# Performance work log

Hardware: AMD Instinct MI355X
Metric: run time of the kernel (lower is better)

## Reference

```python
import jax, jax.numpy as jnp
import numpy as np

DELTA = 0.1
NEG_INF = -1e30


def setup_inputs() -> dict:
    key = jax.random.key(0)
    k1, k2, k3, k4 = jax.random.split(key, 4)
    Bs, Bt, D, C = 8192, 8192, 64, 10
    return {
        "src_feas": jax.random.normal(k1, (Bs, D), dtype=jnp.float32),
        "src_labels": jax.random.randint(k2, (Bs,), 0, C, dtype=jnp.int32),
        "tgt_feas": jax.random.normal(k3, (Bt, D), dtype=jnp.float32),
        "tgt_logits": jax.random.normal(k4, (Bt, C), dtype=jnp.float32),
    }


def reference(src_feas, src_labels, tgt_feas, tgt_logits):
    # The original builds the explicit list of positive pairs (i_tgt, j_src)
    # where tgt sample i is 'confident' (top1-top2 logit gap >= delta) and
    # src_labels[j] == argmax(tgt_logits[i]).  The [P, P] score matrix it
    # forms is s[k, l] = src_feas[j_k] . tgt_feas[i_l], which only depends on
    # (j_k, i_l), so sum(diag(log_softmax(s))) collapses to a weighted
    # logsumexp over the [Bs, Bt] cross-domain score matrix. Same math,
    # fully vectorized, order-invariant.
    Bs = src_feas.shape[0]
    C = tgt_logits.shape[1]

    top2 = jax.lax.top_k(tgt_logits, 2)[0]                  # [Bt, 2]
    conf = (top2[:, 0] - top2[:, 1]) >= DELTA               # [Bt]
    cls = jnp.argmax(tgt_logits, axis=1)                    # [Bt]

    # per-class count of source samples
    counts = jnp.zeros((C,), jnp.float32).at[src_labels].add(1.0)  # [C]
    # w[i] = multiplicity of tgt sample i in the pair list
    w = jnp.where(conf, counts[cls], 0.0)                   # [Bt]

    M = src_feas @ tgt_feas.T                               # [Bs, Bt]
    logw = jnp.where(w > 0, jnp.log(jnp.maximum(w, 1.0)), NEG_INF)
    # L[j] = log sum over all pairs l of exp(M[j, i_l])
    L = jax.scipy.special.logsumexp(M + logw[None, :], axis=1)  # [Bs]

    pair_mask = conf[None, :] & (src_labels[:, None] == cls[None, :])  # [Bs, Bt]
    nce_sum = jnp.sum(jnp.where(pair_mask, M - L[:, None], 0.0))
    P = jnp.sum(w)                                          # total pair count
    nce = nce_sum / (-1.0 * Bs * P)
    return nce
```

## Files before the change

kernel.cpp:

```cpp
#include <hip/hip_runtime.h>
#include <hip/hip_bf16.h>

#define BSZ 8192
#define BTZ 8192
#define DD 64
#define NC 10
#define SHIFT2 20.0f
#define LN2 0.69314718055994531f
#define LOG2E 1.44269504088896341f

typedef __attribute__((ext_vector_type(8))) short bf16x8;
typedef __attribute__((ext_vector_type(4))) float f32x4;

#if defined(__has_builtin)
#if __has_builtin(__builtin_amdgcn_exp2f)
#define EXP2(x) __builtin_amdgcn_exp2f(x)
#else
#define EXP2(x) exp2f(x)
#endif
#else
#define EXP2(x) exp2f(x)
#endif

__device__ __forceinline__ unsigned short f2bf_rne(float f) {
    unsigned int u = __float_as_uint(f);
    u += 0x7FFFu + ((u >> 16) & 1u);
    return (unsigned short)(u >> 16);
}

__global__ __launch_bounds__(256) void kAB(
    const float4* __restrict__ src4, const float4* __restrict__ tgt4,
    const int* __restrict__ labels, const float* __restrict__ logits,
    ushort4* __restrict__ srcb, ushort4* __restrict__ tgtb,
    float* __restrict__ S, float* __restrict__ counts,
    float* __restrict__ cc_part, unsigned char* __restrict__ cls8,
    float* __restrict__ cbias_c, int* __restrict__ cidx,
    int* __restrict__ gcursor)
{
    int t = threadIdx.x;
    if (blockIdx.x < 512) {
        int tid = blockIdx.x * 256 + t;
        float4 s = src4[tid];
        ushort4 os;
        os.x = f2bf_rne(s.x * LOG2E); os.y = f2bf_rne(s.y * LOG2E);
        os.z = f2bf_rne(s.z * LOG2E); os.w = f2bf_rne(s.w * LOG2E);
        srcb[tid] = os;
        float4 v = tgt4[tid];
        ushort4 ot; ot.x = f2bf_rne(v.x); ot.y = f2bf_rne(v.y);
        ot.z = f2bf_rne(v.z); ot.w = f2bf_rne(v.w);
        tgtb[tid] = ot;
        return;
    }
    __shared__ float lcnt[NC];
    __shared__ float hist[NC];
    __shared__ float hred[4][NC];
    __shared__ int lpos;
    __shared__ int lbase;
    int b = blockIdx.x - 512;
    int i = b * 256 + t;
    int w = t >> 6, lane = t & 63;

    float c10[NC];
    #pragma unroll
    for (int c = 0; c < NC; ++c) c10[c] = 0.0f;
    for (int k = 0; k < 32; ++k) {
        int lab = labels[t + 256 * k];
        #pragma unroll
        for (int c = 0; c < NC; ++c) c10[c] += (lab == c) ? 1.0f : 0.0f;
    }
    #pragma unroll
    for (int c = 0; c < NC; ++c) {
        float v = c10[c];
        #pragma unroll
        for (int m = 1; m < 64; m <<= 1) v += __shfl_xor(v, m);
        if (lane == 0) hred[w][c] = v;
    }
    if (t == 0) lpos = 0;
    if (t < NC) hist[t] = 0.0f;
    __syncthreads();
    if (t < NC) lcnt[t] = hred[0][t] + hred[1][t] + hred[2][t] + hred[3][t];
    __syncthreads();
    if (b == 0 && t < NC) counts[t] = lcnt[t];

    float m1 = -3.0e38f, m2 = -3.0e38f; int cls = 0;
    #pragma unroll
    for (int c = 0; c < NC; ++c) {
        float v = logits[i * NC + c];
        if (v > m1) { m2 = m1; m1 = v; cls = c; }
        else if (v > m2) { m2 = v; }
    }
    bool conf = (m1 - m2) >= 0.1f;
    float cnt = lcnt[cls];
    bool live = conf && (cnt > 0.0f);
    cls8[i] = live ? (unsigned char)cls : (unsigned char)255;
    S[i] = 0.0f;
    if (conf) atomicAdd(&hist[cls], 1.0f);
    int myp = 0;
    if (live) myp = atomicAdd(&lpos, 1);
    __syncthreads();
    if (t < NC) cc_part[b * NC + t] = hist[t];
    if (t == 0) lbase = atomicAdd(gcursor, lpos);
    __syncthreads();
    if (live) {
        cidx[lbase + myp] = i;
        cbias_c[lbase + myp] = log2f(cnt) - SHIFT2;
    }
}

__global__ __launch_bounds__(256) void kC(
    const unsigned short* __restrict__ srcb, const unsigned short* __restrict__ tgtb,
    const float* __restrict__ cbias_c, const int* __restrict__ cidx,
    const int* __restrict__ gcursor, float* __restrict__ S,
    const float* __restrict__ srcf, const float* __restrict__ tgtf,
    const int* __restrict__ labels, const unsigned char* __restrict__ cls8,
    float* __restrict__ SC, float* __restrict__ T)
{
    int t = threadIdx.x;
    if (blockIdx.x >= 2048) {
        int bb = blockIdx.x - 2048;
        bool isT = bb >= 32;
        int rb = (bb & 31) * 256;
        const float* F = isT ? tgtf : srcf;
        int w = t >> 6, lane = t & 63;
        float acc[NC];
        #pragma unroll
        for (int c = 0; c < NC; ++c) acc[c] = 0.0f;
        int row0 = rb + w * 64;
        for (int r = 0; r < 64; ++r) {
            int row = row0 + r;
            int lab = isT ? (int)cls8[row] : labels[row];
            float f = F[row * DD + lane];
            #pragma unroll
            for (int c = 0; c < NC; ++c) acc[c] += (lab == c) ? f : 0.0f;
        }
        float* OUT = isT ? T : SC;
        #pragma unroll
        for (int c = 0; c < NC; ++c) atomicAdd(&OUT[c * DD + lane], acc[c]);
        return;
    }

    __shared__ float lds[4][64];
    int w = t >> 6;
    int lane = t & 63;
    int l15 = lane & 15;
    int quad = lane >> 4;
    int colchunk = blockIdx.x & 15;
    int rowg = blockIdx.x >> 4;
    int row_base = rowg * 64;
    int Pn = *gcursor;
    if (colchunk * 512 >= Pn) return;

    bf16x8 a[4][2];
    #pragma unroll
    for (int mb = 0; mb < 4; ++mb) {
        const bf16x8* p = (const bf16x8*)(srcb + (size_t)(row_base + mb * 16 + l15) * DD + quad * 8);
        a[mb][0] = p[0];
        a[mb][1] = p[4];
    }

    float rs[4][4];
    #pragma unroll
    for (int mb = 0; mb < 4; ++mb)
        #pragma unroll
        for (int r = 0; r < 4; ++r) rs[mb][r] = 0.0f;

    int col0 = colchunk * 512 + w * 128;
    #pragma unroll 2
    for (int ct = 0; ct < 8; ++ct) {
        int cb = col0 + ct * 16;
        int cc = cb + l15;
        bool ok = cc < Pn;
        int col = ok ? cidx[cc] : 0;
        float cb2 = ok ? cbias_c[cc] : -1.0e30f;
        const bf16x8* q = (const bf16x8*)(tgtb + (size_t)col * DD + quad * 8);
        bf16x8 b0 = q[0];
        bf16x8 b1 = q[4];
        #pragma unroll
        for (int mb = 0; mb < 4; ++mb) {
            f32x4 acc = {cb2, cb2, cb2, cb2};
            acc = __builtin_amdgcn_mfma_f32_16x16x32_bf16(a[mb][0], b0, acc, 0, 0, 0);
            acc = __builtin_amdgcn_mfma_f32_16x16x32_bf16(a[mb][1], b1, acc, 0, 0, 0);
            #pragma unroll
            for (int r = 0; r < 4; ++r)
                rs[mb][r] += EXP2(acc[r]);
        }
    }

    #pragma unroll
    for (int mb = 0; mb < 4; ++mb) {
        #pragma unroll
        for (int r = 0; r < 4; ++r) {
            float v = rs[mb][r];
            v += __shfl_xor(v, 1);
            v += __shfl_xor(v, 2);
            v += __shfl_xor(v, 4);
            v += __shfl_xor(v, 8);
            if (l15 == 0) lds[w][mb * 16 + quad * 4 + r] = v;
        }
    }
    __syncthreads();
    if (t < 64)
        atomicAdd(&S[row_base + t], lds[0][t] + lds[1][t] + lds[2][t] + lds[3][t]);
}

__global__ __launch_bounds__(256) void kD(
    const float* __restrict__ S, const int* __restrict__ labels,
    const float* __restrict__ counts, const float* __restrict__ cc_part,
    const float* __restrict__ SC, const float* __restrict__ T,
    float* __restrict__ gACC, int* __restrict__ gcnt,
    float* __restrict__ out)
{
    __shared__ float cc[NC];
    __shared__ float redL[4], red1[4], redP[4];
    __shared__ int isLast;
    int t = threadIdx.x;
    int w = t >> 6, lane = t & 63;
    if (t < NC) {
        float s = 0.0f;
        #pragma unroll
        for (int k = 0; k < 32; ++k) s += cc_part[k * NC + t];
        cc[t] = s;
    }
    __syncthreads();
    int j = blockIdx.x * 256 + t;
    float L = (log2f(S[j]) + SHIFT2) * LN2;
    float tl = cc[labels[j]] * L;
    #pragma unroll
    for (int m = 1; m < 64; m <<= 1) tl += __shfl_xor(tl, m);
    if (lane == 0) redL[w] = tl;
    __syncthreads();
    if (t == 0) {
        float v = redL[0] + redL[1] + redL[2] + redL[3];
        atomicAdd(&gACC[0], v);
        __threadfence();
        int old = atomicAdd(gcnt, 1);
        isLast = (old == 31) ? 1 : 0;
    }
    __syncthreads();
    if (!isLast) return;

    float t1 = 0.0f;
    for (int o = t; o < NC * DD; o += 256) t1 += SC[o] * T[o];
    float Pp = (t < NC) ? counts[t] * cc[t] : 0.0f;
    #pragma unroll
    for (int m = 1; m < 64; m <<= 1) {
        t1 += __shfl_xor(t1, m);
        Pp += __shfl_xor(Pp, m);
    }
    if (lane == 0) { red1[w] = t1; redP[w] = Pp; }
    __syncthreads();
    if (t == 0) {
        float term1 = red1[0] + red1[1] + red1[2] + red1[3];
        float P = redP[0] + redP[1] + redP[2] + redP[3];
        float termL = atomicAdd(&gACC[0], 0.0f);
        out[0] = (term1 - termL) / (-(float)BSZ * P);
    }
}

extern "C" void kernel_launch(void* const* d_in, const int* in_sizes, int n_in,
                              void* d_out, int out_size, void* d_ws, size_t ws_size,
                              hipStream_t stream) {
    const float* src    = (const float*)d_in[0];
    const int*   labels = (const int*)d_in[1];
    const float* tgt    = (const float*)d_in[2];
    const float* logits = (const float*)d_in[3];

    char* ws = (char*)d_ws;
    float* S        = (float*)(ws + 0);
    int*   gcursor  = (int*)(ws + 32768);
    int*   gcnt     = (int*)(ws + 32772);
    float* gACC     = (float*)(ws + 32776);
    float* counts   = (float*)(ws + 32784);
    float* cc_part  = (float*)(ws + 32832);
    float* SC       = (float*)(ws + 34112);
    float* T        = (float*)(ws + 36672);
    float* cbias_c  = (float*)(ws + 40960);
    int*   cidx     = (int*)(ws + 73728);
    unsigned char* cls8 = (unsigned char*)(ws + 106496);
    unsigned short* srcb = (unsigned short*)(ws + 114688);
    unsigned short* tgtb = (unsigned short*)(ws + 114688 + 1048576);

    hipMemsetAsync(ws + 32768, 0, 8192, stream);
    kAB<<<544, 256, 0, stream>>>((const float4*)src, (const float4*)tgt, labels,
                                 logits, (ushort4*)srcb, (ushort4*)tgtb,
                                 S, counts, cc_part, cls8, cbias_c, cidx, gcursor);
    kC<<<2112, 256, 0, stream>>>(srcb, tgtb, cbias_c, cidx, gcursor, S,
                                 src, tgt, labels, cls8, SC, T);
    kD<<<32, 256, 0, stream>>>(S, labels, counts, cc_part, SC, T,
                               gACC, gcnt, (float*)d_out);
}
```

Before: 122.1 us.

## Replace compacted column list with dense per-column bias masking in score kernel

Drops the atomic compaction of confident target indices and instead writes a per-column log2 bias for every target, using -1e30 for dead columns. The score kernel then walks all 8192 columns contiguously with no index gather, preloads its B fragments and biases up front, and halves the per-block column chunk, which doubles the grid. Launch bounds now request 4 blocks per CU. This removes the gather indirection, the global cursor read and the serial atomic cursor, but it evaluates exp2 on non-confident columns that were skipped before.

```diff
diff --git a/kernel.cpp b/kernel.cpp
--- a/kernel.cpp
+++ b/kernel.cpp
@@ -34,8 +34,7 @@
     ushort4* __restrict__ srcb, ushort4* __restrict__ tgtb,
     float* __restrict__ S, float* __restrict__ counts,
     float* __restrict__ cc_part, unsigned char* __restrict__ cls8,
-    float* __restrict__ cbias_c, int* __restrict__ cidx,
-    int* __restrict__ gcursor)
+    float* __restrict__ colbias)
 {
     int t = threadIdx.x;
     if (blockIdx.x < 512) {
@@ -54,8 +53,6 @@
     __shared__ float lcnt[NC];
     __shared__ float hist[NC];
     __shared__ float hred[4][NC];
-    __shared__ int lpos;
-    __shared__ int lbase;
     int b = blockIdx.x - 512;
     int i = b * 256 + t;
     int w = t >> 6, lane = t & 63;
@@ -75,7 +72,6 @@
         for (int m = 1; m < 64; m <<= 1) v += __shfl_xor(v, m);
         if (lane == 0) hred[w][c] = v;
     }
-    if (t == 0) lpos = 0;
     if (t < NC) hist[t] = 0.0f;
     __syncthreads();
     if (t < NC) lcnt[t] = hred[0][t] + hred[1][t] + hred[2][t] + hred[3][t];
@@ -92,32 +88,24 @@
     bool conf = (m1 - m2) >= 0.1f;
     float cnt = lcnt[cls];
     bool live = conf && (cnt > 0.0f);
+    colbias[i] = live ? (log2f(cnt) - SHIFT2) : -1.0e30f;
     cls8[i] = live ? (unsigned char)cls : (unsigned char)255;
     S[i] = 0.0f;
     if (conf) atomicAdd(&hist[cls], 1.0f);
-    int myp = 0;
-    if (live) myp = atomicAdd(&lpos, 1);
     __syncthreads();
     if (t < NC) cc_part[b * NC + t] = hist[t];
-    if (t == 0) lbase = atomicAdd(gcursor, lpos);
-    __syncthreads();
-    if (live) {
-        cidx[lbase + myp] = i;
-        cbias_c[lbase + myp] = log2f(cnt) - SHIFT2;
-    }
-}
-
-__global__ __launch_bounds__(256) void kC(
+}
+
+__global__ __launch_bounds__(256, 4) void kC(
     const unsigned short* __restrict__ srcb, const unsigned short* __restrict__ tgtb,
-    const float* __restrict__ cbias_c, const int* __restrict__ cidx,
-    const int* __restrict__ gcursor, float* __restrict__ S,
+    const float* __restrict__ colbias, float* __restrict__ S,
     const float* __restrict__ srcf, const float* __restrict__ tgtf,
     const int* __restrict__ labels, const unsigned char* __restrict__ cls8,
     float* __restrict__ SC, float* __restrict__ T)
 {
     int t = threadIdx.x;
-    if (blockIdx.x >= 2048) {
-        int bb = blockIdx.x - 2048;
+    if (blockIdx.x >= 4096) {
+        int bb = blockIdx.x - 4096;
         bool isT = bb >= 32;
         int rb = (bb & 31) * 256;
         const float* F = isT ? tgtf : srcf;
@@ -144,11 +132,9 @@
     int lane = t & 63;
     int l15 = lane & 15;
     int quad = lane >> 4;
-    int colchunk = blockIdx.x & 15;
-    int rowg = blockIdx.x >> 4;
+    int colchunk = blockIdx.x & 31;
+    int rowg = blockIdx.x >> 5;
     int row_base = rowg * 64;
-    int Pn = *gcursor;
-    if (colchunk * 512 >= Pn) return;
 
     bf16x8 a[4][2];
     #pragma unroll
@@ -157,6 +143,17 @@
         a[mb][0] = p[0];
         a[mb][1] = p[4];
     }
+    int col0 = colchunk * 256 + w * 64;
+    bf16x8 b[4][2];
+    float cb2[4];
+    #pragma unroll
+    for (int ct = 0; ct < 4; ++ct) {
+        int cc = col0 + ct * 16 + l15;
+        const bf16x8* q = (const bf16x8*)(tgtb + (size_t)cc * DD + quad * 8);
+        b[ct][0] = q[0];
+        b[ct][1] = q[4];
+        cb2[ct] = colbias[cc];
+    }
 
     float rs[4][4];
     #pragma unroll
@@ -164,22 +161,13 @@
         #pragma unroll
         for (int r = 0; r < 4; ++r) rs[mb][r] = 0.0f;
 
-    int col0 = colchunk * 512 + w * 128;
-    #pragma unroll 2
-    for (int ct = 0; ct < 8; ++ct) {
-        int cb = col0 + ct * 16;
-        int cc = cb + l15;
-        bool ok = cc < Pn;
-        int col = ok ? cidx[cc] : 0;
-        float cb2 = ok ? cbias_c[cc] : -1.0e30f;
-        const bf16x8* q = (const bf16x8*)(tgtb + (size_t)col * DD + quad * 8);
-        bf16x8 b0 = q[0];
-        bf16x8 b1 = q[4];
+    #pragma unroll
+    for (int ct = 0; ct < 4; ++ct) {
         #pragma unroll
         for (int mb = 0; mb < 4; ++mb) {
-            f32x4 acc = {cb2, cb2, cb2, cb2};
-            acc = __builtin_amdgcn_mfma_f32_16x16x32_bf16(a[mb][0], b0, acc, 0, 0, 0);
-            acc = __builtin_amdgcn_mfma_f32_16x16x32_bf16(a[mb][1], b1, acc, 0, 0, 0);
+            f32x4 acc = {cb2[ct], cb2[ct], cb2[ct], cb2[ct]};
+            acc = __builtin_amdgcn_mfma_f32_16x16x32_bf16(a[mb][0], b[ct][0], acc, 0, 0, 0);
+            acc = __builtin_amdgcn_mfma_f32_16x16x32_bf16(a[mb][1], b[ct][1], acc, 0, 0, 0);
             #pragma unroll
             for (int r = 0; r < 4; ++r)
                 rs[mb][r] += EXP2(acc[r]);
@@ -267,24 +255,22 @@
 
     char* ws = (char*)d_ws;
     float* S        = (float*)(ws + 0);
-    int*   gcursor  = (int*)(ws + 32768);
-    int*   gcnt     = (int*)(ws + 32772);
+    int*   gcnt     = (int*)(ws + 32768);
     float* gACC     = (float*)(ws + 32776);
     float* counts   = (float*)(ws + 32784);
     float* cc_part  = (float*)(ws + 32832);
     float* SC       = (float*)(ws + 34112);
     float* T        = (float*)(ws + 36672);
-    float* cbias_c  = (float*)(ws + 40960);
-    int*   cidx     = (int*)(ws + 73728);
-    unsigned char* cls8 = (unsigned char*)(ws + 106496);
-    unsigned short* srcb = (unsigned short*)(ws + 114688);
-    unsigned short* tgtb = (unsigned short*)(ws + 114688 + 1048576);
+    float* colbias  = (float*)(ws + 40960);
+    unsigned char* cls8 = (unsigned char*)(ws + 73728);
+    unsigned short* srcb = (unsigned short*)(ws + 81920);
+    unsigned short* tgtb = (unsigned short*)(ws + 81920 + 1048576);
 
     hipMemsetAsync(ws + 32768, 0, 8192, stream);
     kAB<<<544, 256, 0, stream>>>((const float4*)src, (const float4*)tgt, labels,
                                  logits, (ushort4*)srcb, (ushort4*)tgtb,
-                                 S, counts, cc_part, cls8, cbias_c, cidx, gcursor);
-    kC<<<2112, 256, 0, stream>>>(srcb, tgtb, cbias_c, cidx, gcursor, S,
+                                 S, counts, cc_part, cls8, colbias);
+    kC<<<4160, 256, 0, stream>>>(srcb, tgtb, colbias, S,
                                  src, tgt, labels, cls8, SC, T);
     kD<<<32, 256, 0, stream>>>(S, labels, counts, cc_part, SC, T,
                                gACC, gcnt, (float*)d_out);
```

New measurement: 123.9 us. About the same (+1.4%).

## Fuse finalization into GEMM kernel and compute positive-pair term from MFMA scores

Applied to the files above, without the earlier changes.

Removes the compacted confident-column list and instead runs the bf16 MFMA logsumexp over all 8192 target columns, masking dead columns with a large negative bias stored alongside the class in a packed per-column metadata array. The positive-pair sum is accumulated inside the MFMA loop by comparing row labels to column classes, which replaces the separate class-sum feature reduction blocks. The final reduction now runs in the last-finishing block of the GEMM kernel, which drops the third launch and the memset. In exchange every column is always computed, so the early-exit skip for chunks beyond the live count is gone, the inner loop gains a compare and add per element, and the positive term now uses bf16 scores with a bias correction instead of fp32 feature sums.

```diff
diff --git a/kernel.cpp b/kernel.cpp
--- a/kernel.cpp
+++ b/kernel.cpp
@@ -33,9 +33,8 @@
     const int* __restrict__ labels, const float* __restrict__ logits,
     ushort4* __restrict__ srcb, ushort4* __restrict__ tgtb,
     float* __restrict__ S, float* __restrict__ counts,
-    float* __restrict__ cc_part, unsigned char* __restrict__ cls8,
-    float* __restrict__ cbias_c, int* __restrict__ cidx,
-    int* __restrict__ gcursor)
+    float* __restrict__ cc_part, int2* __restrict__ colmeta,
+    int* __restrict__ gcnt, float* __restrict__ gACC)
 {
     int t = threadIdx.x;
     if (blockIdx.x < 512) {
@@ -54,8 +53,6 @@
     __shared__ float lcnt[NC];
     __shared__ float hist[NC];
     __shared__ float hred[4][NC];
-    __shared__ int lpos;
-    __shared__ int lbase;
     int b = blockIdx.x - 512;
     int i = b * 256 + t;
     int w = t >> 6, lane = t & 63;
@@ -75,12 +72,15 @@
         for (int m = 1; m < 64; m <<= 1) v += __shfl_xor(v, m);
         if (lane == 0) hred[w][c] = v;
     }
-    if (t == 0) lpos = 0;
     if (t < NC) hist[t] = 0.0f;
     __syncthreads();
     if (t < NC) lcnt[t] = hred[0][t] + hred[1][t] + hred[2][t] + hred[3][t];
     __syncthreads();
-    if (b == 0 && t < NC) counts[t] = lcnt[t];
+    if (b == 0) {
+        if (t < NC) counts[t] = lcnt[t];
+        if (t == 64) *gcnt = 0;
+        if (t == 65) gACC[0] = 0.0f;
+    }
 
     float m1 = -3.0e38f, m2 = -3.0e38f; int cls = 0;
     #pragma unroll
@@ -92,54 +92,28 @@
     bool conf = (m1 - m2) >= 0.1f;
     float cnt = lcnt[cls];
     bool live = conf && (cnt > 0.0f);
-    cls8[i] = live ? (unsigned char)cls : (unsigned char)255;
+    float cb2 = live ? (log2f(cnt) - SHIFT2) : -1.0e30f;
+    colmeta[i] = make_int2(__float_as_int(cb2), live ? cls : 255);
     S[i] = 0.0f;
     if (conf) atomicAdd(&hist[cls], 1.0f);
-    int myp = 0;
-    if (live) myp = atomicAdd(&lpos, 1);
     __syncthreads();
     if (t < NC) cc_part[b * NC + t] = hist[t];
-    if (t == 0) lbase = atomicAdd(gcursor, lpos);
-    __syncthreads();
-    if (live) {
-        cidx[lbase + myp] = i;
-        cbias_c[lbase + myp] = log2f(cnt) - SHIFT2;
-    }
 }
 
 __global__ __launch_bounds__(256) void kC(
     const unsigned short* __restrict__ srcb, const unsigned short* __restrict__ tgtb,
-    const float* __restrict__ cbias_c, const int* __restrict__ cidx,
-    const int* __restrict__ gcursor, float* __restrict__ S,
-    const float* __restrict__ srcf, const float* __restrict__ tgtf,
-    const int* __restrict__ labels, const unsigned char* __restrict__ cls8,
-    float* __restrict__ SC, float* __restrict__ T)
+    const int2* __restrict__ colmeta, const int* __restrict__ labels,
+    float* __restrict__ S, const float* __restrict__ counts,
+    const float* __restrict__ cc_part,
+    float* __restrict__ gACC, int* __restrict__ gcnt,
+    float* __restrict__ out)
 {
+    __shared__ float lds[4][64];
+    __shared__ float t1red[4];
+    __shared__ int isLast;
+    __shared__ float ccs[NC];
+    __shared__ float redv[4];
     int t = threadIdx.x;
-    if (blockIdx.x >= 2048) {
-        int bb = blockIdx.x - 2048;
-        bool isT = bb >= 32;
-        int rb = (bb & 31) * 256;
-        const float* F = isT ? tgtf : srcf;
-        int w = t >> 6, lane = t & 63;
-        float acc[NC];
-        #pragma unroll
-        for (int c = 0; c < NC; ++c) acc[c] = 0.0f;
-        int row0 = rb + w * 64;
-        for (int r = 0; r < 64; ++r) {
-            int row = row0 + r;
-            int lab = isT ? (int)cls8[row] : labels[row];
-            float f = F[row * DD + lane];
-            #pragma unroll
-            for (int c = 0; c < NC; ++c) acc[c] += (lab == c) ? f : 0.0f;
-        }
-        float* OUT = isT ? T : SC;
-        #pragma unroll
-        for (int c = 0; c < NC; ++c) atomicAdd(&OUT[c * DD + lane], acc[c]);
-        return;
-    }
-
-    __shared__ float lds[4][64];
     int w = t >> 6;
     int lane = t & 63;
     int l15 = lane & 15;
@@ -147,15 +121,16 @@
     int colchunk = blockIdx.x & 15;
     int rowg = blockIdx.x >> 4;
     int row_base = rowg * 64;
-    int Pn = *gcursor;
-    if (colchunk * 512 >= Pn) return;
 
     bf16x8 a[4][2];
+    int rlp[4];
     #pragma unroll
     for (int mb = 0; mb < 4; ++mb) {
         const bf16x8* p = (const bf16x8*)(srcb + (size_t)(row_base + mb * 16 + l15) * DD + quad * 8);
         a[mb][0] = p[0];
         a[mb][1] = p[4];
+        int4 rl = ((const int4*)labels)[(row_base + mb * 16 + quad * 4) >> 2];
+        rlp[mb] = (rl.x & 255) | ((rl.y & 255) << 8) | ((rl.z & 255) << 16) | ((rl.w & 255) << 24);
     }
 
     float rs[4][4];
@@ -163,26 +138,29 @@
     for (int mb = 0; mb < 4; ++mb)
         #pragma unroll
         for (int r = 0; r < 4; ++r) rs[mb][r] = 0.0f;
+    float t1p = 0.0f;
 
     int col0 = colchunk * 512 + w * 128;
     #pragma unroll 2
     for (int ct = 0; ct < 8; ++ct) {
-        int cb = col0 + ct * 16;
-        int cc = cb + l15;
-        bool ok = cc < Pn;
-        int col = ok ? cidx[cc] : 0;
-        float cb2 = ok ? cbias_c[cc] : -1.0e30f;
-        const bf16x8* q = (const bf16x8*)(tgtb + (size_t)col * DD + quad * 8);
+        int ci = col0 + ct * 16 + l15;
+        const bf16x8* q = (const bf16x8*)(tgtb + (size_t)ci * DD + quad * 8);
         bf16x8 b0 = q[0];
         bf16x8 b1 = q[4];
+        int2 meta = colmeta[ci];
+        float cb2 = __int_as_float(meta.x);
+        int ccls = meta.y;
         #pragma unroll
         for (int mb = 0; mb < 4; ++mb) {
             f32x4 acc = {cb2, cb2, cb2, cb2};
             acc = __builtin_amdgcn_mfma_f32_16x16x32_bf16(a[mb][0], b0, acc, 0, 0, 0);
             acc = __builtin_amdgcn_mfma_f32_16x16x32_bf16(a[mb][1], b1, acc, 0, 0, 0);
             #pragma unroll
-            for (int r = 0; r < 4; ++r)
-                rs[mb][r] += EXP2(acc[r]);
+            for (int r = 0; r < 4; ++r) {
+                float e = acc[r];
+                rs[mb][r] += EXP2(e);
+                t1p += (((rlp[mb] >> (8 * r)) & 255) == ccls) ? e : 0.0f;
+            }
         }
     }
 
@@ -198,62 +176,53 @@
             if (l15 == 0) lds[w][mb * 16 + quad * 4 + r] = v;
         }
     }
+    #pragma unroll
+    for (int m = 1; m < 64; m <<= 1) t1p += __shfl_xor(t1p, m);
+    if (lane == 0) t1red[w] = t1p;
     __syncthreads();
     if (t < 64)
         atomicAdd(&S[row_base + t], lds[0][t] + lds[1][t] + lds[2][t] + lds[3][t]);
-}
-
-__global__ __launch_bounds__(256) void kD(
-    const float* __restrict__ S, const int* __restrict__ labels,
-    const float* __restrict__ counts, const float* __restrict__ cc_part,
-    const float* __restrict__ SC, const float* __restrict__ T,
-    float* __restrict__ gACC, int* __restrict__ gcnt,
-    float* __restrict__ out)
-{
-    __shared__ float cc[NC];
-    __shared__ float redL[4], red1[4], redP[4];
-    __shared__ int isLast;
-    int t = threadIdx.x;
-    int w = t >> 6, lane = t & 63;
+    if (t == 0) {
+        atomicAdd(&gACC[0], t1red[0] + t1red[1] + t1red[2] + t1red[3]);
+        __threadfence();
+        int old = atomicAdd(gcnt, 1);
+        isLast = (old == 2047) ? 1 : 0;
+    }
+    __syncthreads();
+    if (!isLast) return;
+
+    __threadfence();
     if (t < NC) {
         float s = 0.0f;
         #pragma unroll
         for (int k = 0; k < 32; ++k) s += cc_part[k * NC + t];
-        cc[t] = s;
-    }
-    __syncthreads();
-    int j = blockIdx.x * 256 + t;
-    float L = (log2f(S[j]) + SHIFT2) * LN2;
-    float tl = cc[labels[j]] * L;
-    #pragma unroll
-    for (int m = 1; m < 64; m <<= 1) tl += __shfl_xor(tl, m);
-    if (lane == 0) redL[w] = tl;
+        ccs[t] = s;
+    }
+    __syncthreads();
+    float acc2 = 0.0f;
+    for (int j = t; j < BSZ; j += 256) {
+        float Sj = __hip_atomic_load(&S[j], __ATOMIC_RELAXED, __HIP_MEMORY_SCOPE_AGENT);
+        float L = (log2f(Sj) + SHIFT2) * LN2;
+        acc2 -= ccs[labels[j]] * L;
+    }
+    #pragma unroll
+    for (int m = 1; m < 64; m <<= 1) acc2 += __shfl_xor(acc2, m);
+    if (lane == 0) redv[w] = acc2;
     __syncthreads();
     if (t == 0) {
-        float v = redL[0] + redL[1] + redL[2] + redL[3];
-        atomicAdd(&gACC[0], v);
-        __threadfence();
-        int old = atomicAdd(gcnt, 1);
-        isLast = (old == 31) ? 1 : 0;
-    }
-    __syncthreads();
-    if (!isLast) return;
-
-    float t1 = 0.0f;
-    for (int o = t; o < NC * DD; o += 256) t1 += SC[o] * T[o];
-    float Pp = (t < NC) ? counts[t] * cc[t] : 0.0f;
-    #pragma unroll
-    for (int m = 1; m < 64; m <<= 1) {
-        t1 += __shfl_xor(t1, m);
-        Pp += __shfl_xor(Pp, m);
-    }
-    if (lane == 0) { red1[w] = t1; redP[w] = Pp; }
-    __syncthreads();
-    if (t == 0) {
-        float term1 = red1[0] + red1[1] + red1[2] + red1[3];
-        float P = redP[0] + redP[1] + redP[2] + redP[3];
-        float termL = atomicAdd(&gACC[0], 0.0f);
-        out[0] = (term1 - termL) / (-(float)BSZ * P);
+        float negL = redv[0] + redv[1] + redv[2] + redv[3];
+        float t1sum = __hip_atomic_load(&gACC[0], __ATOMIC_RELAXED, __HIP_MEMORY_SCOPE_AGENT);
+        float corr = 0.0f, P = 0.0f;
+        #pragma unroll
+        for (int c = 0; c < NC; ++c) {
+            float n = counts[c];
+            if (n > 0.0f) {
+                corr += ccs[c] * n * (log2f(n) - SHIFT2);
+                P += n * ccs[c];
+            }
+        }
+        float term1 = (t1sum - corr) * LN2;
+        out[0] = (term1 + negL) / (-(float)BSZ * P);
     }
 }
 
@@ -267,25 +236,17 @@
 
     char* ws = (char*)d_ws;
     float* S        = (float*)(ws + 0);
-    int*   gcursor  = (int*)(ws + 32768);
-    int*   gcnt     = (int*)(ws + 32772);
-    float* gACC     = (float*)(ws + 32776);
-    float* counts   = (float*)(ws + 32784);
-    float* cc_part  = (float*)(ws + 32832);
-    float* SC       = (float*)(ws + 34112);
-    float* T        = (float*)(ws + 36672);
-    float* cbias_c  = (float*)(ws + 40960);
-    int*   cidx     = (int*)(ws + 73728);
-    unsigned char* cls8 = (unsigned char*)(ws + 106496);
+    float* counts   = (float*)(ws + 32768);
+    int*   gcnt     = (int*)(ws + 32832);
+    float* gACC     = (float*)(ws + 32896);
+    float* cc_part  = (float*)(ws + 32960);
+    int2*  colmeta  = (int2*)(ws + 40960);
     unsigned short* srcb = (unsigned short*)(ws + 114688);
     unsigned short* tgtb = (unsigned short*)(ws + 114688 + 1048576);
 
-    hipMemsetAsync(ws + 32768, 0, 8192, stream);
     kAB<<<544, 256, 0, stream>>>((const float4*)src, (const float4*)tgt, labels,
                                  logits, (ushort4*)srcb, (ushort4*)tgtb,
-                                 S, counts, cc_part, cls8, cbias_c, cidx, gcursor);
-    kC<<<2112, 256, 0, stream>>>(srcb, tgtb, cbias_c, cidx, gcursor, S,
-                                 src, tgt, labels, cls8, SC, T);
-    kD<<<32, 256, 0, stream>>>(S, labels, counts, cc_part, SC, T,
-                               gACC, gcnt, (float*)d_out);
-}
+                                 S, counts, cc_part, colmeta, gcnt, gACC);
+    kC<<<2048, 256, 0, stream>>>(srcb, tgtb, colmeta, labels,
+                                 S, counts, cc_part, gACC, gcnt, (float*)d_out);
+}
```

Result: slower. 147.1 us (+20.4%).
